# Performance work log

Measured on AMD Instinct MI355X. Metric: run time of the kernel, lower is better.

Reference implementation:

```python
import jax, jax.numpy as jnp
import numpy as np

NS, NI, NC, C, E, M = 50000, 20000, 1000, 128, 1000000, 250000


def setup_inputs() -> dict:
    key = jax.random.key(0)
    ks = jax.random.split(key, 12)
    xavier = (2.0 / (C + C)) ** 0.5  # xavier_normal_ std for square weight
    return {
        "stu_x": jax.random.normal(ks[0], (NS, C), jnp.float32),
        "item_x": jax.random.normal(ks[1], (NI, C), jnp.float32),
        "conc_x": jax.random.normal(ks[2], (NC, C), jnp.float32),
        "W_stu": jax.random.normal(ks[3], (C, C), jnp.float32) * xavier,
        "b_stu": jnp.zeros((C,), jnp.float32),
        "W_item": jax.random.normal(ks[4], (C, C), jnp.float32) * xavier,
        "b_item": jnp.zeros((C,), jnp.float32),
        "W_pred": jax.random.normal(ks[5], (1, C), jnp.float32) * ((2.0 / (1 + C)) ** 0.5),
        "b_pred": jnp.zeros((1,), jnp.float32),
        "stu_track": jax.random.randint(ks[6], (E,), 0, NS, jnp.int32),
        "item_index": jax.random.randint(ks[7], (E,), 0, NI, jnp.int32),
        "conc_index": jax.random.randint(ks[8], (E,), 0, NC, jnp.int32),
        "mean_index": jax.random.randint(ks[9], (E,), 0, M, jnp.int32),
        "num_segments": M,
    }


def _segment_mean(vals, seg_ids, num_segments):
    sums = jax.ops.segment_sum(vals, seg_ids, num_segments=num_segments)
    cnt = jax.ops.segment_sum(jnp.ones((vals.shape[0], 1), vals.dtype), seg_ids,
                              num_segments=num_segments)
    return sums / jnp.maximum(cnt, 1.0)


def reference(stu_x, item_x, conc_x, W_stu, b_stu, W_item, b_item, W_pred, b_pred,
              stu_track, item_index, conc_index, mean_index, num_segments):
    # Feature (stu): shared lin_l=lin_r; aggregate is identity -> per-edge output
    conc_s = conc_x @ W_stu.T          # [NC, C] projected source (concepts)
    stu_p = stu_x @ W_stu.T            # [NS, C] projected target (students)
    stu_feature = jax.nn.sigmoid(conc_s[conc_index] + stu_p[stu_track] + b_stu)  # [E, C]

    # Feature (item): SparseTensor(row=item, col=conc) -> x_j from conc, x_i from item
    conc_i = conc_x @ W_item.T         # [NC, C]
    item_p = item_x @ W_item.T         # [NI, C]
    item_feature = jax.nn.sigmoid(conc_i[conc_index] + item_p[item_index] + b_item)  # [E, C]

    # scatter-mean of per-edge difference over mean_index groups
    pred_input = _segment_mean(stu_feature - item_feature, mean_index, num_segments)  # [M, C]
    pred = jax.nn.sigmoid(pred_input @ W_pred.T + b_pred)  # [M, 1]
    return pred.reshape(-1)
```

## Files before the change

### kernel.cpp

```cpp
#include <hip/hip_runtime.h>

typedef unsigned short u16;
typedef unsigned int   u32;

typedef short short8 __attribute__((ext_vector_type(8)));
typedef float floatx4 __attribute__((ext_vector_type(4)));

#define CDIM 128
#define K_NEG_LOG2E -1.4426950408889634f
#define CNT_SCALE 16777216.0

#define WLDS_STRIDE 136
#define PACK_BLOCKS 512

__device__ __forceinline__ float bf2f_lo(u32 h) {
    union { u32 u; float f; } v; v.u = h << 16; return v.f;
}
__device__ __forceinline__ float bf2f_hi(u32 h) {
    union { u32 u; float f; } v; v.u = h & 0xffff0000u; return v.f;
}
__device__ __forceinline__ u16 f2bf(float f) {
    union { float f; u32 u; } v; v.f = f;
    u32 u = v.u;
    return (u16)((u + 0x7FFFu + ((u >> 16) & 1u)) >> 16);
}
__device__ __forceinline__ float sig_std(float x) {
    return __builtin_amdgcn_rcpf(1.0f + __builtin_amdgcn_exp2f(x * K_NEG_LOG2E));
}

__device__ __forceinline__ void proj_tile16_lds(
    const float* __restrict__ X, const u16* __restrict__ wlds,
    const float* __restrict__ bias, u16* __restrict__ out,
    int nrows, int ostride, int ooff, int row0, int lane)
{
    const int m = lane & 15;
    const int g = lane >> 4;

    short8 a[4];
    {
        int arow = row0 + m;
        if (arow >= nrows) arow = nrows - 1;
        const float* xrow = X + (size_t)arow * CDIM;
#pragma unroll
        for (int s = 0; s < 4; ++s) {
            float4 f0 = *(const float4*)(xrow + s * 32 + g * 8);
            float4 f1 = *(const float4*)(xrow + s * 32 + g * 8 + 4);
            a[s][0] = (short)f2bf(f0.x); a[s][1] = (short)f2bf(f0.y);
            a[s][2] = (short)f2bf(f0.z); a[s][3] = (short)f2bf(f0.w);
            a[s][4] = (short)f2bf(f1.x); a[s][5] = (short)f2bf(f1.y);
            a[s][6] = (short)f2bf(f1.z); a[s][7] = (short)f2bf(f1.w);
        }
    }

#pragma unroll
    for (int ct = 0; ct < 8; ++ct) {
        const u16* wrow = wlds + (size_t)(ct * 16 + m) * WLDS_STRIDE;
        floatx4 acc = {0.f, 0.f, 0.f, 0.f};
#pragma unroll
        for (int s = 0; s < 4; ++s) {
            short8 b = *(const short8*)(wrow + s * 32 + g * 8);
            acc = __builtin_amdgcn_mfma_f32_16x16x32_bf16(a[s], b, acc, 0, 0, 0);
        }
        const int col = ct * 16 + m;
        const float badd = bias ? bias[col] * K_NEG_LOG2E : 0.f;
#pragma unroll
        for (int i = 0; i < 4; ++i) {
            int r = row0 + g * 4 + i;
            if (r < nrows)
                out[(size_t)r * ostride + ooff + col] =
                    f2bf(__builtin_amdgcn_exp2f(acc[i] + badd));
        }
    }
}

__global__ __launch_bounds__(256) void fused_prep_proj(
    const float* __restrict__ stu_x, const float* __restrict__ item_x,
    const float* __restrict__ conc_x,
    const float* __restrict__ Wstu, const float* __restrict__ Witem,
    const float* __restrict__ b_stu, const float* __restrict__ b_item,
    u16* __restrict__ stu_p, u16* __restrict__ item_p, u16* __restrict__ conc_cat,
    float4* __restrict__ zero4, int nZero4,
    const int* __restrict__ stu_track, const int* __restrict__ item_index,
    const int* __restrict__ conc_index, const int* __restrict__ mean_index,
    int4* __restrict__ idx4, int E,
    int NS, int NI, int NC)
{
    __shared__ u16 wlds[128 * WLDS_STRIDE];

    const int PB0 = (NS + 63) / 64, PB1 = (NI + 63) / 64, PB2 = (NC + 63) / 64;
    const int PBtot = PB0 + PB1 + 2 * PB2;
    int b = blockIdx.x;

    if (b >= PBtot) {
        const int tid = (b - PBtot) * 256 + threadIdx.x;
        const int stride = PACK_BLOCKS * 256;
        const float4 z = {0.f, 0.f, 0.f, 0.f};
        for (int i = tid; i < nZero4; i += stride) zero4[i] = z;
        for (int e = tid; e < E; e += stride) {
            int4 t;
            t.x = stu_track[e]  << 8;
            t.y = item_index[e] << 8;
            t.z = conc_index[e] << 9;
            t.w = mean_index[e] << 3;
            idx4[e] = t;
        }
        return;
    }

    const float* X; const float* Wsel; const float* bias;
    u16* out; int nrows, ostride, ooff, base;
    if (b < PB0)      { X = stu_x;  Wsel = Wstu;  bias = nullptr; out = stu_p;
                        nrows = NS; ostride = 128; ooff = 0;   base = b * 64; }
    else if ((b -= PB0) < PB1)
                      { X = item_x; Wsel = Witem; bias = nullptr; out = item_p;
                        nrows = NI; ostride = 128; ooff = 0;   base = b * 64; }
    else if ((b -= PB1) < PB2)
                      { X = conc_x; Wsel = Wstu;  bias = b_stu;  out = conc_cat;
                        nrows = NC; ostride = 256; ooff = 0;   base = b * 64; }
    else              { b -= PB2;
                        X = conc_x; Wsel = Witem; bias = b_item; out = conc_cat;
                        nrows = NC; ostride = 256; ooff = 128; base = b * 64; }

    {
        const int t   = threadIdx.x;
        const int col = t >> 1;
        const int k0  = (t & 1) * 64;
        const float4* src = (const float4*)(Wsel + col * 128 + k0);
        u32* dst = (u32*)(wlds + col * WLDS_STRIDE + k0);
#pragma unroll
        for (int i = 0; i < 16; ++i) {
            float4 f = src[i];
            dst[2 * i]     = (u32)f2bf(f.x * K_NEG_LOG2E) |
                             ((u32)f2bf(f.y * K_NEG_LOG2E) << 16);
            dst[2 * i + 1] = (u32)f2bf(f.z * K_NEG_LOG2E) |
                             ((u32)f2bf(f.w * K_NEG_LOG2E) << 16);
        }
    }
    __syncthreads();

    const int lane = threadIdx.x & 63;
    const int row0 = base + (threadIdx.x >> 6) * 16;
    if (row0 < nrows)
        proj_tile16_lds(X, wlds, bias, out, nrows, ostride, ooff, row0, lane);
}

__global__ __launch_bounds__(256) void edge_kernel(
    const u16* __restrict__ stu_p, const u16* __restrict__ item_p,
    const u16* __restrict__ conc_cat,
    const int4* __restrict__ idx4,
    const float* __restrict__ w_pred,
    double* __restrict__ sc, int E)
{
    const int lane = threadIdx.x & 63;
    const int sub  = lane & 15;
    const int g    = lane >> 4;
    const int waveId = (int)((blockIdx.x * blockDim.x + threadIdx.x) >> 6);
    const int S      = (int)((gridDim.x * blockDim.x) >> 6);

    const float4 wA = ((const float4*)w_pred)[sub * 2];
    const float4 wB = ((const float4*)w_pred)[sub * 2 + 1];
    float2 w2[4];
    w2[0] = make_float2(wA.x, wA.y); w2[1] = make_float2(wA.z, wA.w);
    w2[2] = make_float2(wB.x, wB.y); w2[3] = make_float2(wB.z, wB.w);
    const u32 lane_off = (u32)sub * 16;

    const int nQuads = (E + 3) >> 2;
    int q = waveId;
    if (q >= nQuads) return;

    auto ldidx = [&](int qq) -> int4 {
        int e = qq * 4 + g;
        e = (e < E) ? e : (E - 1);
        return idx4[e];
    };
    auto compute = [&](const uint4& sv, const uint4& iv,
                       const uint4& ca, const uint4& cb,
                       const int4& I, int qq) {
        const u32 su[4] = {sv.x, sv.y, sv.z, sv.w};
        const u32 iu[4] = {iv.x, iv.y, iv.z, iv.w};
        const u32 au[4] = {ca.x, ca.y, ca.z, ca.w};
        const u32 bu[4] = {cb.x, cb.y, cb.z, cb.w};
        const float2 one = make_float2(1.f, 1.f);
        float2 vacc = make_float2(0.f, 0.f);
#pragma unroll
        for (int j = 0; j < 4; ++j) {
            float2 A  = make_float2(bf2f_lo(au[j]), bf2f_hi(au[j]));
            float2 Sx = make_float2(bf2f_lo(su[j]), bf2f_hi(su[j]));
            float2 B  = make_float2(bf2f_lo(bu[j]), bf2f_hi(bu[j]));
            float2 Ix = make_float2(bf2f_lo(iu[j]), bf2f_hi(iu[j]));
            float2 ea = A * Sx;
            float2 eb = B * Ix;
            float2 den = (ea + one) * (eb + one);
            float2 num = eb - ea;
            float2 rd = make_float2(__builtin_amdgcn_rcpf(den.x),
                                    __builtin_amdgcn_rcpf(den.y));
            vacc += (num * rd) * w2[j];
        }
        float v = vacc.x + vacc.y;
        v += __shfl_xor(v, 1, 64);
        v += __shfl_xor(v, 2, 64);
        v += __shfl_xor(v, 4, 64);
        v += __shfl_xor(v, 8, 64);
        if (sub == 0 && (qq * 4 + g) < E)
            atomicAdd((double*)((char*)sc + (u32)I.w), (double)v + CNT_SCALE);
    };

#define GATH(I_, sv_, iv_, ca_, cb_) { \
        sv_ = *(const uint4*)((const char*)stu_p  + ((u32)(I_).x + lane_off)); \
        iv_ = *(const uint4*)((const char*)item_p + ((u32)(I_).y + lane_off)); \
        const char* cp_ = (const char*)conc_cat + ((u32)(I_).z + lane_off); \
        ca_ = *(const uint4*)cp_; cb_ = *(const uint4*)(cp_ + 256); }

#define STEP(DA, DB, IA, IB, IC) { \
        GATH(I##IB, sv##DB, iv##DB, ca##DB, cb##DB); \
        I##IC = ldidx(q + 2 * S); \
        __builtin_amdgcn_sched_barrier(0); \
        compute(sv##DA, iv##DA, ca##DA, cb##DA, I##IA, q); \
        q += S; \
        if (q >= nQuads) break; }

    int4 I0 = ldidx(q), I1 = ldidx(q + S), I2, I3;
    uint4 sv0, iv0, ca0, cb0, sv1, iv1, ca1, cb1;
    GATH(I0, sv0, iv0, ca0, cb0);

    for (;;) {
        STEP(0, 1, 0, 1, 2)
        STEP(1, 0, 1, 2, 3)
        STEP(0, 1, 2, 3, 0)
        STEP(1, 0, 3, 0, 1)
    }
#undef STEP
#undef GATH
}

__global__ __launch_bounds__(256) void final_kernel(
    const double* __restrict__ sc,
    const float* __restrict__ b_pred, float* __restrict__ out, int M)
{
    const int i = blockIdx.x * blockDim.x + threadIdx.x;
    if (i < M) {
        const double acc = sc[i];
        const double cnt = rint(acc * (1.0 / CNT_SCALE));
        const double sum = acc - cnt * CNT_SCALE;
        const float mean = (float)(sum / fmax(cnt, 1.0));
        out[i] = sig_std(mean + b_pred[0]);
    }
}

extern "C" void kernel_launch(void* const* d_in, const int* in_sizes, int n_in,
                              void* d_out, int out_size, void* d_ws, size_t ws_size,
                              hipStream_t stream) {
    const float* stu_x    = (const float*)d_in[0];
    const float* item_x   = (const float*)d_in[1];
    const float* conc_x   = (const float*)d_in[2];
    const float* W_stu    = (const float*)d_in[3];
    const float* b_stu    = (const float*)d_in[4];
    const float* W_item   = (const float*)d_in[5];
    const float* b_item   = (const float*)d_in[6];
    const float* W_pred   = (const float*)d_in[7];
    const float* b_pred   = (const float*)d_in[8];
    const int* stu_track  = (const int*)d_in[9];
    const int* item_index = (const int*)d_in[10];
    const int* conc_index = (const int*)d_in[11];
    const int* mean_index = (const int*)d_in[12];

    const int NS = in_sizes[0] / CDIM;
    const int NI = in_sizes[1] / CDIM;
    const int NC = in_sizes[2] / CDIM;
    const int E  = in_sizes[9];
    const int M  = out_size;

    double* sc     = (double*)d_ws;
    u16* stu_p     = (u16*)(sc + M);
    u16* item_p    = stu_p  + (size_t)NS * CDIM;
    u16* conc_cat  = item_p + (size_t)NI * CDIM;
    int4* idx4     = (int4*)(conc_cat + (size_t)NC * 256);

    const int nZero4 = (int)(((size_t)M * sizeof(double)) / 16);
    const int PB0 = (NS + 63) / 64, PB1 = (NI + 63) / 64, PB2 = (NC + 63) / 64;
    const int PBtot = PB0 + PB1 + 2 * PB2;

    fused_prep_proj<<<PBtot + PACK_BLOCKS, 256, 0, stream>>>(
        stu_x, item_x, conc_x, W_stu, W_item, b_stu, b_item,
        stu_p, item_p, conc_cat,
        (float4*)sc, nZero4,
        stu_track, item_index, conc_index, mean_index, idx4, E,
        NS, NI, NC);

    edge_kernel<<<4096, 256, 0, stream>>>(stu_p, item_p, conc_cat,
                                          idx4, W_pred, sc, E);

    final_kernel<<<(M + 255) / 256, 256, 0, stream>>>(sc, b_pred, (float*)d_out, M);
}
```

Measured before the change: 196.0 us.

## Deepen gather pipeline: prefetch student/item rows two steps ahead

Restructures the software pipeline in the edge kernel so the per-edge student/item row gathers are issued two iterations ahead and the concept row gathers one iteration ahead, with index loads three iterations ahead. A triple-buffered rotation of registers and a six-step unrolled loop replace the previous double-buffered scheme. The aim is to hide more of the latency of the random global gathers. The cost is extra live registers, which may lower occupancy.

```diff
diff --git a/kernel.cpp b/kernel.cpp
--- a/kernel.cpp
+++ b/kernel.cpp
@@ -175,7 +175,7 @@
     };
     auto compute = [&](const uint4& sv, const uint4& iv,
                        const uint4& ca, const uint4& cb,
-                       const int4& I, int qq) {
+                       u32 mw, int qq) {
         const u32 su[4] = {sv.x, sv.y, sv.z, sv.w};
         const u32 iu[4] = {iv.x, iv.y, iv.z, iv.w};
         const u32 au[4] = {ca.x, ca.y, ca.z, ca.w};
@@ -202,35 +202,44 @@
         v += __shfl_xor(v, 4, 64);
         v += __shfl_xor(v, 8, 64);
         if (sub == 0 && (qq * 4 + g) < E)
-            atomicAdd((double*)((char*)sc + (u32)I.w), (double)v + CNT_SCALE);
+            atomicAdd((double*)((char*)sc + mw), (double)v + CNT_SCALE);
     };
 
-#define GATH(I_, sv_, iv_, ca_, cb_) { \
+#define GATH_S(I_, sv_, iv_) { \
         sv_ = *(const uint4*)((const char*)stu_p  + ((u32)(I_).x + lane_off)); \
-        iv_ = *(const uint4*)((const char*)item_p + ((u32)(I_).y + lane_off)); \
+        iv_ = *(const uint4*)((const char*)item_p + ((u32)(I_).y + lane_off)); }
+#define GATH_C(I_, ca_, cb_) { \
         const char* cp_ = (const char*)conc_cat + ((u32)(I_).z + lane_off); \
         ca_ = *(const uint4*)cp_; cb_ = *(const uint4*)(cp_ + 256); }
 
-#define STEP(DA, DB, IA, IB, IC) { \
-        GATH(I##IB, sv##DB, iv##DB, ca##DB, cb##DB); \
-        I##IC = ldidx(q + 2 * S); \
+#define STEP(SC, CC, IC, ICN1, ICN2, SF, CF) { \
+        const u32 mw = (u32)IC.w; \
+        IC = ldidx(q + 3 * S); \
         __builtin_amdgcn_sched_barrier(0); \
-        compute(sv##DA, iv##DA, ca##DA, cb##DA, I##IA, q); \
+        GATH_C(ICN1, CF##a, CF##b); \
+        GATH_S(ICN2, SF##s, SF##i); \
+        __builtin_amdgcn_sched_barrier(0); \
+        compute(SC##s, SC##i, CC##a, CC##b, mw, q); \
         q += S; \
         if (q >= nQuads) break; }
 
-    int4 I0 = ldidx(q), I1 = ldidx(q + S), I2, I3;
-    uint4 sv0, iv0, ca0, cb0, sv1, iv1, ca1, cb1;
-    GATH(I0, sv0, iv0, ca0, cb0);
+    int4 i0 = ldidx(q), i1 = ldidx(q + S), i2 = ldidx(q + 2 * S);
+    uint4 s0s, s0i, s1s, s1i, s2s, s2i, c0a, c0b, c1a, c1b;
+    GATH_C(i0, c0a, c0b);
+    GATH_S(i0, s0s, s0i);
+    GATH_S(i1, s1s, s1i);
 
     for (;;) {
-        STEP(0, 1, 0, 1, 2)
-        STEP(1, 0, 1, 2, 3)
-        STEP(0, 1, 2, 3, 0)
-        STEP(1, 0, 3, 0, 1)
+        STEP(s0, c0, i0, i1, i2, s2, c1)
+        STEP(s1, c1, i1, i2, i0, s0, c0)
+        STEP(s2, c0, i2, i0, i1, s1, c1)
+        STEP(s0, c1, i0, i1, i2, s2, c0)
+        STEP(s1, c0, i1, i2, i0, s0, c1)
+        STEP(s2, c1, i2, i0, i1, s1, c0)
     }
 #undef STEP
-#undef GATH
+#undef GATH_S
+#undef GATH_C
 }
 
 __global__ __launch_bounds__(256) void final_kernel(
@@ -290,5 +299,5 @@
     edge_kernel<<<4096, 256, 0, stream>>>(stu_p, item_p, conc_cat,
                                           idx4, W_pred, sc, E);
 
-    final_kernel<<<(M + 255) / 256, 256, 0, stream>>>(sc, b_pred, (float*)d_out, M);
-}
+    final_kernel<<<(M + 255) / 256, 0 ? 0 : 256, 0, stream>>>(sc, b_pred, (float*)d_out, M);
+}
```

Measured after the change: 192.6 us. About the same (-1.7%).
